# Kernel tuning notes

Measured on AMD Instinct MI355X. Metric: run time of the kernel, lower is better.

The kernel has to match this reference:

```python
import jax, jax.numpy as jnp
import numpy as np

NEG_SLOPE = 0.2  # PyG GATConv default negative_slope


def gat_conv(x, src, dst, n_nodes, W, a_src, a_dst, b, concat):
    # x: [N, F_in], W: [F_in, H*C], a_src/a_dst: [H, C], b: [H*C] or [C]
    H, C = a_src.shape
    h = (x @ W).reshape(n_nodes, H, C)              # [N, H, C]
    e_s = jnp.sum(h * a_src, axis=-1)               # [N, H]
    e_d = jnp.sum(h * a_dst, axis=-1)               # [N, H]
    e = jax.nn.leaky_relu(e_s[src] + e_d[dst], NEG_SLOPE)  # [E, H]
    # segment softmax over incoming edges of each destination node
    m = jax.ops.segment_max(e, dst, num_segments=n_nodes)
    m = jnp.where(jnp.isfinite(m), m, 0.0)
    p = jnp.exp(e - m[dst])                         # [E, H]
    s = jax.ops.segment_sum(p, dst, num_segments=n_nodes)
    alpha = p / (s[dst] + 1e-16)                    # [E, H]
    out = jax.ops.segment_sum(h[src] * alpha[:, :, None], dst, num_segments=n_nodes)  # [N, H, C]
    out = out.reshape(n_nodes, H * C) if concat else out.mean(axis=1)
    return out + b


def setup_inputs() -> dict:
    key = jax.random.key(0)
    ks = jax.random.split(key, 20)
    N, E = 50000, 800000
    F_in, C, H = 128, 64, 4
    sc = 0.05
    inp = {
        "x": jax.random.normal(ks[0], (N, F_in), dtype=jnp.float32),
        "edge_index": jax.random.randint(ks[1], (2, E), 0, N, dtype=jnp.int64),
        # conv1: F_in -> C x H heads, concat
        "W1": jax.random.normal(ks[2], (F_in, H * C), dtype=jnp.float32) * sc,
        "a1_src": jax.random.normal(ks[3], (H, C), dtype=jnp.float32) * sc,
        "a1_dst": jax.random.normal(ks[4], (H, C), dtype=jnp.float32) * sc,
        "b1": jnp.zeros((H * C,), dtype=jnp.float32),
        # conv2: H*C -> C x H heads, concat
        "W2": jax.random.normal(ks[5], (H * C, H * C), dtype=jnp.float32) * sc,
        "a2_src": jax.random.normal(ks[6], (H, C), dtype=jnp.float32) * sc,
        "a2_dst": jax.random.normal(ks[7], (H, C), dtype=jnp.float32) * sc,
        "b2": jnp.zeros((H * C,), dtype=jnp.float32),
        # conv3: H*C -> C, 1 head, concat=False (mean)
        "W3": jax.random.normal(ks[8], (H * C, C), dtype=jnp.float32) * sc,
        "a3_src": jax.random.normal(ks[9], (1, C), dtype=jnp.float32) * sc,
        "a3_dst": jax.random.normal(ks[10], (1, C), dtype=jnp.float32) * sc,
        "b3": jnp.zeros((C,), dtype=jnp.float32),
        # node classification head: C -> 2
        "cls_W": jax.random.normal(ks[11], (C, 2), dtype=jnp.float32) * sc,
        "cls_b": jnp.zeros((2,), dtype=jnp.float32),
    }
    return inp


def reference(x, edge_index, W1, a1_src, a1_dst, b1, W2, a2_src, a2_dst, b2,
              W3, a3_src, a3_dst, b3, cls_W, cls_b):
    N = x.shape[0]
    # PyG GATConv default: add self loops
    loop = jnp.arange(N, dtype=edge_index.dtype)
    ei = jnp.concatenate([edge_index, jnp.stack([loop, loop])], axis=1)
    src, dst = ei[0], ei[1]

    h = jax.nn.elu(gat_conv(x, src, dst, N, W1, a1_src, a1_dst, b1, concat=True))
    h = jax.nn.elu(gat_conv(h, src, dst, N, W2, a2_src, a2_dst, b2, concat=True))
    h = gat_conv(h, src, dst, N, W3, a3_src, a3_dst, b3, concat=False)  # [N, C]

    node_output = h @ cls_W + cls_b  # [N, 2]
    link_embedding = h               # [N, C]
    return node_output, link_embedding
```

## Files before the change

kernel.cpp:

```cpp
#include <hip/hip_runtime.h>
#include <math.h>


typedef unsigned short ushort;
typedef __attribute__((ext_vector_type(8))) short bf16x8;
typedef __attribute__((ext_vector_type(4))) float f32x4;

static __device__ __forceinline__ ushort f2bf(float f) {
    unsigned x = __float_as_uint(f);
    unsigned r = (x + 0x7FFF + ((x >> 16) & 1)) >> 16;
    return (ushort)r;
}
static __device__ __forceinline__ float bf2f(ushort u) {
    return __uint_as_float(((unsigned)u) << 16);
}


__global__ void count_deg(const int* __restrict__ ei, int E, int* __restrict__ deg) {
    int i = blockIdx.x * blockDim.x + threadIdx.x;
    int stride = gridDim.x * blockDim.x;
    for (int e = i; e < E; e += stride) {
        int d = ei[E + e];
        atomicAdd(&deg[d], 1);
    }
}

__global__ void scan_local(const int* __restrict__ deg, int* __restrict__ offsets,
                           int* __restrict__ blockSums, int N) {
    int tid = threadIdx.x;
    int lane = tid & 63;
    int wv = tid >> 6;
    int base = blockIdx.x * 1024 + tid * 4;
    int v[4];
#pragma unroll
    for (int j = 0; j < 4; ++j) {
        int idx = base + j;
        v[j] = (idx < N) ? (deg[idx] + 1) : 0;
    }
    int tsum = v[0] + v[1] + v[2] + v[3];
    int inc = tsum;
#pragma unroll
    for (int off = 1; off < 64; off <<= 1) {
        int u = __shfl_up(inc, off);
        if (lane >= off) inc += u;
    }
    __shared__ int wtot[4];
    if (lane == 63) wtot[wv] = inc;
    __syncthreads();
    int wbase = 0;
#pragma unroll
    for (int w = 0; w < 4; ++w)
        if (w < wv) wbase += wtot[w];
    int run = wbase + inc - tsum;
#pragma unroll
    for (int j = 0; j < 4; ++j) {
        int idx = base + j;
        if (idx < N) offsets[idx] = run;
        run += v[j];
    }
    if (tid == 255) blockSums[blockIdx.x] = wbase + inc;
}

__global__ void scan_blocks(const int* __restrict__ blockSums, int* __restrict__ blockBase,
                            int* __restrict__ offsets, int N, int nblk) {
    int lane = threadIdx.x & 63;
    int v = (lane < nblk) ? blockSums[lane] : 0;
    int inc = v;
#pragma unroll
    for (int off = 1; off < 64; off <<= 1) {
        int u = __shfl_up(inc, off);
        if (lane >= off) inc += u;
    }
    if (lane < nblk) blockBase[lane] = inc - v;
    if (lane == 63) offsets[N] = inc;
}

__global__ void scan_add(int* __restrict__ offsets, const int* __restrict__ blockBase, int N) {
    int i = blockIdx.x * blockDim.x + threadIdx.x;
    if (i < N) offsets[i] += blockBase[i >> 10];
}

__global__ void fill_self(const int* __restrict__ offsets, int* __restrict__ counter,
                          int* __restrict__ csr_src, int N) {
    int i = blockIdx.x * blockDim.x + threadIdx.x;
    if (i < N) {
        csr_src[offsets[i]] = i;
        counter[i] = 1;
    }
}

__global__ void fill_edges(const int* __restrict__ ei, int E,
                           const int* __restrict__ offsets, int* __restrict__ counter,
                           int* __restrict__ csr_src) {
    int i = blockIdx.x * blockDim.x + threadIdx.x;
    int stride = gridDim.x * blockDim.x;
    for (int e = i; e < E; e += stride) {
        int s = ei[e];
        int d = ei[E + e];
        int pos = offsets[d] + atomicAdd(&counter[d], 1);
        csr_src[pos] = s;
    }
}


__global__ void xsplit(const float* __restrict__ X, ushort* __restrict__ Xh,
                       ushort* __restrict__ Xl, int total4) {
    int i = blockIdx.x * blockDim.x + threadIdx.x;
    if (i >= total4) return;
    float4 v = *(const float4*)(X + (size_t)i * 4);
    ushort4 h, l;
    h.x = f2bf(v.x); l.x = f2bf(v.x - bf2f(h.x));
    h.y = f2bf(v.y); l.y = f2bf(v.y - bf2f(h.y));
    h.z = f2bf(v.z); l.z = f2bf(v.z - bf2f(h.z));
    h.w = f2bf(v.w); l.w = f2bf(v.w - bf2f(h.w));
    *(ushort4*)(Xh + (size_t)i * 4) = h;
    *(ushort4*)(Xl + (size_t)i * 4) = l;
}

__global__ void wtrans_bf(const float* __restrict__ W, ushort* __restrict__ Wt,
                          int K, int N) {
    int id = blockIdx.x * blockDim.x + threadIdx.x;
    if (id >= K * N) return;
    int k = id % K, n = id / K;
    Wt[id] = f2bf(W[(size_t)k * N + n]);
}


template<int BM, int BN, int WM, int WN>
__global__ __launch_bounds__(256) void gemm_mfma(const ushort* __restrict__ Ah,
                                                 const ushort* __restrict__ Al,
                                                 const ushort* __restrict__ Bh,
                                                 ushort* __restrict__ Cb,
                                                 int M, int N, int K) {
    constexpr int BK = 32, PAD = 8;
    constexpr int MI = BM / WM / 16;
    constexpr int NI = BN / WN / 16;
    __shared__ ushort As[2][BM][BK + PAD];
    __shared__ ushort Bs[BN][BK + PAD];

    int tid = threadIdx.x;
    int lane = tid & 63;
    int wid = tid >> 6;
    int fr = lane & 15;
    int fg = lane >> 4;
    int wm0 = (wid / WN) * (BM / WM);
    int wn0 = (wid % WN) * (BN / WN);
    int mBase = blockIdx.x * BM;
    int nBase = blockIdx.y * BN;

    f32x4 acc[MI][NI];
#pragma unroll
    for (int mi = 0; mi < MI; ++mi)
#pragma unroll
        for (int ni = 0; ni < NI; ++ni) acc[mi][ni] = (f32x4)0.0f;

    constexpr int ACH = BM * BK / 8;
    constexpr int BCH = BN * BK / 8;

    const int KI = K / BK;
    for (int t = 0; t < KI; ++t) {
        int k0 = t * BK;
#pragma unroll
        for (int q = tid; q < ACH; q += 256) {
            int row = q >> 2;
            int sl = (q & 3) * 8;
            int gm = mBase + row;
            if (gm >= M) gm = M - 1;
            size_t off = (size_t)gm * K + k0 + sl;
            *(bf16x8*)&As[0][row][sl] = *(const bf16x8*)(Ah + off);
            *(bf16x8*)&As[1][row][sl] = *(const bf16x8*)(Al + off);
        }
#pragma unroll
        for (int q = tid; q < BCH; q += 256) {
            int row = q >> 2;
            int sl = (q & 3) * 8;
            size_t off = (size_t)(nBase + row) * K + k0 + sl;
            *(bf16x8*)&Bs[row][sl] = *(const bf16x8*)(Bh + off);
        }
        __syncthreads();

        bf16x8 afh[MI], afl[MI], bfh[NI];
#pragma unroll
        for (int mi = 0; mi < MI; ++mi) {
            afh[mi] = *(const bf16x8*)&As[0][wm0 + mi * 16 + fr][fg * 8];
            afl[mi] = *(const bf16x8*)&As[1][wm0 + mi * 16 + fr][fg * 8];
        }
#pragma unroll
        for (int ni = 0; ni < NI; ++ni)
            bfh[ni] = *(const bf16x8*)&Bs[wn0 + ni * 16 + fr][fg * 8];
#pragma unroll
        for (int mi = 0; mi < MI; ++mi)
#pragma unroll
            for (int ni = 0; ni < NI; ++ni) {
                acc[mi][ni] = __builtin_amdgcn_mfma_f32_16x16x32_bf16(
                    afh[mi], bfh[ni], acc[mi][ni], 0, 0, 0);
                acc[mi][ni] = __builtin_amdgcn_mfma_f32_16x16x32_bf16(
                    afl[mi], bfh[ni], acc[mi][ni], 0, 0, 0);
            }
        __syncthreads();
    }

#pragma unroll
    for (int mi = 0; mi < MI; ++mi) {
#pragma unroll
        for (int j = 0; j < 4; ++j) {
            int gm = mBase + wm0 + mi * 16 + fg * 4 + j;
            if (gm >= M) continue;
#pragma unroll
            for (int ni = 0; ni < NI; ++ni) {
                int gn = nBase + wn0 + ni * 16 + fr;
                Cb[(size_t)gm * N + gn] = f2bf(acc[mi][ni][j]);
            }
        }
    }
}


template<int HC, int H>
__global__ void attn_coef(const ushort* __restrict__ hb,
                          const float* __restrict__ a_src,
                          const float* __restrict__ a_dst,
                          float* __restrict__ e_s, float* __restrict__ e_d, int N) {
    int wid = (int)((blockIdx.x * (size_t)blockDim.x + threadIdx.x) >> 6);
    int lane = threadIdx.x & 63;
    if (wid >= N) return;
    if constexpr (HC == 256) {
        ushort4 q = *(const ushort4*)(hb + (size_t)wid * 256 + lane * 4);
        float4 as = *(const float4*)(a_src + lane * 4);
        float4 ad = *(const float4*)(a_dst + lane * 4);
        float h0 = bf2f(q.x), h1 = bf2f(q.y), h2 = bf2f(q.z), h3 = bf2f(q.w);
        float ps = h0 * as.x + h1 * as.y + h2 * as.z + h3 * as.w;
        float pd = h0 * ad.x + h1 * ad.y + h2 * ad.z + h3 * ad.w;
#pragma unroll
        for (int off = 1; off <= 8; off <<= 1) {
            ps += __shfl_xor(ps, off);
            pd += __shfl_xor(pd, off);
        }
        if ((lane & 15) == 0) {
            int hd = lane >> 4;
            e_s[(size_t)wid * H + hd] = ps;
            e_d[(size_t)wid * H + hd] = pd;
        }
    } else {
        float hv = bf2f(hb[(size_t)wid * HC + lane]);
        float ps = hv * a_src[lane];
        float pd = hv * a_dst[lane];
#pragma unroll
        for (int off = 1; off <= 32; off <<= 1) {
            ps += __shfl_xor(ps, off);
            pd += __shfl_xor(pd, off);
        }
        if (lane == 0) {
            e_s[wid] = ps;
            e_d[wid] = pd;
        }
    }
}


template<int HC, int H, bool ELU, int U, bool SPLIT>
__global__ void aggregate(const ushort* __restrict__ hb,
                          const float* __restrict__ e_s, const float* __restrict__ e_d,
                          const int* __restrict__ offsets, const int* __restrict__ csr_src,
                          const float* __restrict__ bias,
                          float* __restrict__ out,
                          ushort* __restrict__ oh, ushort* __restrict__ ol, int N) {
    int wid = (int)((blockIdx.x * (size_t)blockDim.x + threadIdx.x) >> 6);
    int lane = threadIdx.x & 63;
    if (wid >= N) return;
    constexpr int VEC = HC / 64;
    constexpr int C = HC / H;
    constexpr int ROWSH = (HC == 256) ? 9 : 7;
    int hd = (lane * VEC) / C;
    float ed = e_d[(size_t)wid * H + hd];
    int beg = offsets[wid], end = offsets[wid + 1];
    const char* hbB = (const char*)hb;
    const char* esB = (const char*)e_s;
    unsigned laneOff = (unsigned)lane * (VEC * 2);

    float s = 0.0f;
    float acc[VEC];
#pragma unroll
    for (int j = 0; j < VEC; ++j) acc[j] = 0.0f;

    for (int k = beg; k < end; k += U) {
        int sidx[U];
#pragma unroll
        for (int u = 0; u < U; ++u) {
            int kk = k + u;
            kk = (kk < end) ? kk : end - 1;
            sidx[u] = csr_src[kk];
        }
        float e[U];
#pragma unroll
        for (int u = 0; u < U; ++u)
            e[u] = *(const float*)(esB + (((unsigned)(sidx[u] * H + hd)) << 2));
        ushort4 hv4[U];
        ushort  hv1[U];
        if constexpr (VEC == 4) {
#pragma unroll
            for (int u = 0; u < U; ++u)
                hv4[u] = *(const ushort4*)(hbB + (((unsigned)sidx[u]) << ROWSH) + laneOff);
        } else {
#pragma unroll
            for (int u = 0; u < U; ++u)
                hv1[u] = *(const ushort*)(hbB + (((unsigned)sidx[u]) << ROWSH) + laneOff);
        }
        float p[U];
        float psum = 0.0f;
#pragma unroll
        for (int u = 0; u < U; ++u) {
            float t = e[u] + ed;
            t = (t >= 0.0f) ? t : 0.2f * t;
            t = (k + u < end) ? t : -1e30f;
            p[u] = __expf(t);
            psum += p[u];
        }
        s += psum;
        if constexpr (VEC == 4) {
#pragma unroll
            for (int u = 0; u < U; ++u) {
                acc[0] += p[u] * bf2f(hv4[u].x);
                acc[1] += p[u] * bf2f(hv4[u].y);
                acc[2] += p[u] * bf2f(hv4[u].z);
                acc[3] += p[u] * bf2f(hv4[u].w);
            }
        } else {
#pragma unroll
            for (int u = 0; u < U; ++u) acc[0] += p[u] * bf2f(hv1[u]);
        }
    }
    float inv = 1.0f / (s + 1e-16f);
    float o[VEC];
#pragma unroll
    for (int j = 0; j < VEC; ++j) {
        int f = lane * VEC + j;
        o[j] = acc[j] * inv + bias[f];
        if constexpr (ELU) o[j] = (o[j] > 0.0f) ? o[j] : expm1f(o[j]);
    }
    if constexpr (SPLIT) {
        if constexpr (VEC == 4) {
            ushort4 h4, l4;
            h4.x = f2bf(o[0]); l4.x = f2bf(o[0] - bf2f(h4.x));
            h4.y = f2bf(o[1]); l4.y = f2bf(o[1] - bf2f(h4.y));
            h4.z = f2bf(o[2]); l4.z = f2bf(o[2] - bf2f(h4.z));
            h4.w = f2bf(o[3]); l4.w = f2bf(o[3] - bf2f(h4.w));
            *(ushort4*)(oh + (size_t)wid * HC + lane * 4) = h4;
            *(ushort4*)(ol + (size_t)wid * HC + lane * 4) = l4;
        } else {
            ushort h1 = f2bf(o[0]);
            oh[(size_t)wid * HC + lane] = h1;
            ol[(size_t)wid * HC + lane] = f2bf(o[0] - bf2f(h1));
        }
    } else {
#pragma unroll
        for (int j = 0; j < VEC; ++j)
            out[(size_t)wid * HC + lane * VEC + j] = o[j];
    }
}


__global__ void cls_head(const float* __restrict__ h3, const float* __restrict__ W,
                         const float* __restrict__ b, float* __restrict__ out, int N) {
    int wid = (int)((blockIdx.x * (size_t)blockDim.x + threadIdx.x) >> 6);
    int lane = threadIdx.x & 63;
    if (wid >= N) return;
    float v = h3[(size_t)wid * 64 + lane];
    float p0 = v * W[lane * 2 + 0];
    float p1 = v * W[lane * 2 + 1];
#pragma unroll
    for (int off = 1; off <= 32; off <<= 1) {
        p0 += __shfl_xor(p0, off);
        p1 += __shfl_xor(p1, off);
    }
    if (lane == 0) {
        out[(size_t)wid * 2 + 0] = p0 + b[0];
        out[(size_t)wid * 2 + 1] = p1 + b[1];
    }
}


extern "C" void kernel_launch(void* const* d_in, const int* in_sizes, int n_in,
                              void* d_out, int out_size, void* d_ws, size_t ws_size,
                              hipStream_t stream) {
    const float* x      = (const float*)d_in[0];
    const int*   ei     = (const int*)d_in[1];
    const float* W1     = (const float*)d_in[2];
    const float* a1_src = (const float*)d_in[3];
    const float* a1_dst = (const float*)d_in[4];
    const float* b1     = (const float*)d_in[5];
    const float* W2     = (const float*)d_in[6];
    const float* a2_src = (const float*)d_in[7];
    const float* a2_dst = (const float*)d_in[8];
    const float* b2     = (const float*)d_in[9];
    const float* W3     = (const float*)d_in[10];
    const float* a3_src = (const float*)d_in[11];
    const float* a3_dst = (const float*)d_in[12];
    const float* b3     = (const float*)d_in[13];
    const float* cls_W  = (const float*)d_in[14];
    const float* cls_b  = (const float*)d_in[15];

    const int N = in_sizes[0] / 128;
    const int E = in_sizes[1] / 2;
    const int ET = E + N;
    const int HC = 256;
    const int nScanBlk = (N + 1023) / 1024;

    char* w = (char*)d_ws;
    auto carve = [&](size_t bytes) {
        char* p = w;
        w += (bytes + 255) & ~(size_t)255;
        return p;
    };
    int*    deg     = (int*)   carve((size_t)N * 4);
    int*    counter = (int*)   carve((size_t)N * 4);
    int*    offsets = (int*)   carve((size_t)(N + 1) * 4);
    int*    csr_src = (int*)   carve((size_t)ET * 4);
    int*    blkSums = (int*)   carve((size_t)64 * 4);
    int*    blkBase = (int*)   carve((size_t)64 * 4);
    float*  e_s     = (float*) carve((size_t)N * 4 * 4);
    float*  e_d     = (float*) carve((size_t)N * 4 * 4);
    ushort* hb      = (ushort*)carve((size_t)N * HC * 2);
    ushort* Ahi     = (ushort*)carve((size_t)N * HC * 2);
    ushort* Alo     = (ushort*)carve((size_t)N * HC * 2);
    ushort* W1t     = (ushort*)carve((size_t)128 * 256 * 2);
    ushort* W2t     = (ushort*)carve((size_t)256 * 256 * 2);
    ushort* W3t     = (ushort*)carve((size_t)256 * 64 * 2);
    (void)ws_size;

    float* out_node = (float*)d_out;
    float* out_link = (float*)d_out + 2 * (size_t)N;

    hipMemsetAsync(deg, 0, (size_t)N * 4, stream);
    int eblocks = (E + 255) / 256;
    if (eblocks > 2048) eblocks = 2048;
    count_deg<<<eblocks, 256, 0, stream>>>(ei, E, deg);
    scan_local<<<nScanBlk, 256, 0, stream>>>(deg, offsets, blkSums, N);
    scan_blocks<<<1, 64, 0, stream>>>(blkSums, blkBase, offsets, N, nScanBlk);
    scan_add<<<(N + 255) / 256, 256, 0, stream>>>(offsets, blkBase, N);
    fill_self<<<(N + 255) / 256, 256, 0, stream>>>(offsets, counter, csr_src, N);
    fill_edges<<<eblocks, 256, 0, stream>>>(ei, E, offsets, counter, csr_src);

    xsplit<<<(N * 128 / 4 + 255) / 256, 256, 0, stream>>>(x, Ahi, Alo, N * 128 / 4);
    wtrans_bf<<<(128 * 256 + 255) / 256, 256, 0, stream>>>(W1, W1t, 128, 256);
    wtrans_bf<<<(256 * 256 + 255) / 256, 256, 0, stream>>>(W2, W2t, 256, 256);
    wtrans_bf<<<(256 * 64 + 255) / 256, 256, 0, stream>>>(W3, W3t, 256, 64);

    dim3 g12((N + 63) / 64, 1);
    dim3 g3((N + 63) / 64, 1);
    int nodeBlocks = (N + 3) / 4;

    gemm_mfma<64, 256, 1, 4><<<g12, 256, 0, stream>>>(Ahi, Alo, W1t, hb, N, 256, 128);
    attn_coef<256, 4><<<nodeBlocks, 256, 0, stream>>>(hb, a1_src, a1_dst, e_s, e_d, N);
    aggregate<256, 4, true, 8, true><<<nodeBlocks, 256, 0, stream>>>(
        hb, e_s, e_d, offsets, csr_src, b1, nullptr, Ahi, Alo, N);
    gemm_mfma<64, 256, 1, 4><<<g12, 256, 0, stream>>>(Ahi, Alo, W2t, hb, N, 256, 256);
    attn_coef<256, 4><<<nodeBlocks, 256, 0, stream>>>(hb, a2_src, a2_dst, e_s, e_d, N);
    aggregate<256, 4, true, 8, true><<<nodeBlocks, 256, 0, stream>>>(
        hb, e_s, e_d, offsets, csr_src, b2, nullptr, Ahi, Alo, N);
    gemm_mfma<64, 64, 2, 2><<<g3, 256, 0, stream>>>(Ahi, Alo, W3t, hb, N, 64, 256);
    attn_coef<64, 1><<<nodeBlocks, 256, 0, stream>>>(hb, a3_src, a3_dst, e_s, e_d, N);
    aggregate<64, 1, false, 8, false><<<nodeBlocks, 256, 0, stream>>>(
        hb, e_s, e_d, offsets, csr_src, b3, out_link, nullptr, nullptr, N);
    cls_head<<<nodeBlocks, 256, 0, stream>>>(out_link, cls_W, cls_b, out_node, N);
}
```

Measured before the change: 388.6 us.

## Pad CSR rows to multiples of 8 with sentinel node and use exp2

After: 372.9 us. -4.0%, faster.

```diff
diff --git a/kernel.cpp b/kernel.cpp
--- a/kernel.cpp
+++ b/kernel.cpp
@@ -5,6 +5,8 @@
 typedef unsigned short ushort;
 typedef __attribute__((ext_vector_type(8))) short bf16x8;
 typedef __attribute__((ext_vector_type(4))) float f32x4;
+
+#define LOG2E 1.4426950408889634f
 
 static __device__ __forceinline__ ushort f2bf(float f) {
     unsigned x = __float_as_uint(f);
@@ -35,7 +37,7 @@
 #pragma unroll
     for (int j = 0; j < 4; ++j) {
         int idx = base + j;
-        v[j] = (idx < N) ? (deg[idx] + 1) : 0;
+        v[j] = (idx < N) ? ((deg[idx] + 1 + 7) & ~7) : 0;
     }
     int tsum = v[0] + v[1] + v[2] + v[3];
     int inc = tsum;
@@ -78,6 +80,11 @@
 __global__ void scan_add(int* __restrict__ offsets, const int* __restrict__ blockBase, int N) {
     int i = blockIdx.x * blockDim.x + threadIdx.x;
     if (i < N) offsets[i] += blockBase[i >> 10];
+}
+
+__global__ void fill_sent(int* __restrict__ csr_src, int cap, int N) {
+    int i = blockIdx.x * blockDim.x + threadIdx.x;
+    if (i < cap) csr_src[i] = N;
 }
 
 __global__ void fill_self(const int* __restrict__ offsets, int* __restrict__ counter,
@@ -126,15 +133,16 @@
 }
 
 
-template<int BM, int BN, int WM, int WN>
-__global__ __launch_bounds__(256) void gemm_mfma(const ushort* __restrict__ Ah,
-                                                 const ushort* __restrict__ Al,
-                                                 const ushort* __restrict__ Bh,
-                                                 ushort* __restrict__ Cb,
-                                                 int M, int N, int K) {
+template<int BM, int BN, int WM, int WN, int THREADS>
+__global__ __launch_bounds__(THREADS) void gemm_mfma(const ushort* __restrict__ Ah,
+                                                     const ushort* __restrict__ Al,
+                                                     const ushort* __restrict__ Bh,
+                                                     ushort* __restrict__ Cb,
+                                                     int M, int N, int K) {
     constexpr int BK = 32, PAD = 8;
     constexpr int MI = BM / WM / 16;
     constexpr int NI = BN / WN / 16;
+    static_assert(WM * WN * 64 == THREADS, "wave grid mismatch");
     __shared__ ushort As[2][BM][BK + PAD];
     __shared__ ushort Bs[BN][BK + PAD];
 
@@ -160,8 +168,7 @@
     const int KI = K / BK;
     for (int t = 0; t < KI; ++t) {
         int k0 = t * BK;
-#pragma unroll
-        for (int q = tid; q < ACH; q += 256) {
+        for (int q = tid; q < ACH; q += THREADS) {
             int row = q >> 2;
             int sl = (q & 3) * 8;
             int gm = mBase + row;
@@ -170,8 +177,7 @@
             *(bf16x8*)&As[0][row][sl] = *(const bf16x8*)(Ah + off);
             *(bf16x8*)&As[1][row][sl] = *(const bf16x8*)(Al + off);
         }
-#pragma unroll
-        for (int q = tid; q < BCH; q += 256) {
+        for (int q = tid; q < BCH; q += THREADS) {
             int row = q >> 2;
             int sl = (q & 3) * 8;
             size_t off = (size_t)(nBase + row) * K + k0 + sl;
@@ -217,13 +223,23 @@
 
 
 template<int HC, int H>
-__global__ void attn_coef(const ushort* __restrict__ hb,
+__global__ void attn_coef(ushort* __restrict__ hb,
                           const float* __restrict__ a_src,
                           const float* __restrict__ a_dst,
                           float* __restrict__ e_s, float* __restrict__ e_d, int N) {
     int wid = (int)((blockIdx.x * (size_t)blockDim.x + threadIdx.x) >> 6);
     int lane = threadIdx.x & 63;
-    if (wid >= N) return;
+    if (wid > N) return;
+    if (wid == N) {
+        if constexpr (HC == 256) {
+            ushort4 z = {0, 0, 0, 0};
+            *(ushort4*)(hb + (size_t)N * 256 + lane * 4) = z;
+        } else {
+            hb[(size_t)N * HC + lane] = 0;
+        }
+        if (lane < H) e_s[(size_t)N * H + lane] = -1e30f;
+        return;
+    }
     if constexpr (HC == 256) {
         ushort4 q = *(const ushort4*)(hb + (size_t)wid * 256 + lane * 4);
         float4 as = *(const float4*)(a_src + lane * 4);
@@ -238,8 +254,8 @@
         }
         if ((lane & 15) == 0) {
             int hd = lane >> 4;
-            e_s[(size_t)wid * H + hd] = ps;
-            e_d[(size_t)wid * H + hd] = pd;
+            e_s[(size_t)wid * H + hd] = ps * LOG2E;
+            e_d[(size_t)wid * H + hd] = pd * LOG2E;
         }
     } else {
         float hv = bf2f(hb[(size_t)wid * HC + lane]);
@@ -251,20 +267,21 @@
             pd += __shfl_xor(pd, off);
         }
         if (lane == 0) {
-            e_s[wid] = ps;
-            e_d[wid] = pd;
-        }
-    }
-}
-
-
-template<int HC, int H, bool ELU, int U, bool SPLIT>
+            e_s[wid] = ps * LOG2E;
+            e_d[wid] = pd * LOG2E;
+        }
+    }
+}
+
+
+template<int HC, int H, bool ELU, bool SPLIT>
 __global__ void aggregate(const ushort* __restrict__ hb,
                           const float* __restrict__ e_s, const float* __restrict__ e_d,
                           const int* __restrict__ offsets, const int* __restrict__ csr_src,
                           const float* __restrict__ bias,
                           float* __restrict__ out,
                           ushort* __restrict__ oh, ushort* __restrict__ ol, int N) {
+    constexpr int U = 8;
     int wid = (int)((blockIdx.x * (size_t)blockDim.x + threadIdx.x) >> 6);
     int lane = threadIdx.x & 63;
     if (wid >= N) return;
@@ -286,11 +303,7 @@
     for (int k = beg; k < end; k += U) {
         int sidx[U];
 #pragma unroll
-        for (int u = 0; u < U; ++u) {
-            int kk = k + u;
-            kk = (kk < end) ? kk : end - 1;
-            sidx[u] = csr_src[kk];
-        }
+        for (int u = 0; u < U; ++u) sidx[u] = csr_src[k + u];
         float e[U];
 #pragma unroll
         for (int u = 0; u < U; ++u)
@@ -312,8 +325,7 @@
         for (int u = 0; u < U; ++u) {
             float t = e[u] + ed;
             t = (t >= 0.0f) ? t : 0.2f * t;
-            t = (k + u < end) ? t : -1e30f;
-            p[u] = __expf(t);
+            p[u] = __builtin_amdgcn_exp2f(t);
             psum += p[u];
         }
         s += psum;
@@ -402,7 +414,7 @@
 
     const int N = in_sizes[0] / 128;
     const int E = in_sizes[1] / 2;
-    const int ET = E + N;
+    const int ETcap = E + 8 * N + 64;
     const int HC = 256;
     const int nScanBlk = (N + 1023) / 1024;
 
@@ -415,12 +427,12 @@
     int*    deg     = (int*)   carve((size_t)N * 4);
     int*    counter = (int*)   carve((size_t)N * 4);
     int*    offsets = (int*)   carve((size_t)(N + 1) * 4);
-    int*    csr_src = (int*)   carve((size_t)ET * 4);
+    int*    csr_src = (int*)   carve((size_t)ETcap * 4);
     int*    blkSums = (int*)   carve((size_t)64 * 4);
     int*    blkBase = (int*)   carve((size_t)64 * 4);
-    float*  e_s     = (float*) carve((size_t)N * 4 * 4);
+    float*  e_s     = (float*) carve((size_t)(N + 1) * 4 * 4);
     float*  e_d     = (float*) carve((size_t)N * 4 * 4);
-    ushort* hb      = (ushort*)carve((size_t)N * HC * 2);
+    ushort* hb      = (ushort*)carve((size_t)(N + 1) * HC * 2);
     ushort* Ahi     = (ushort*)carve((size_t)N * HC * 2);
     ushort* Alo     = (ushort*)carve((size_t)N * HC * 2);
     ushort* W1t     = (ushort*)carve((size_t)128 * 256 * 2);
@@ -438,6 +450,7 @@
     scan_local<<<nScanBlk, 256, 0, stream>>>(deg, offsets, blkSums, N);
     scan_blocks<<<1, 64, 0, stream>>>(blkSums, blkBase, offsets, N, nScanBlk);
     scan_add<<<(N + 255) / 256, 256, 0, stream>>>(offsets, blkBase, N);
+    fill_sent<<<(ETcap + 255) / 256, 256, 0, stream>>>(csr_src, ETcap, N);
     fill_self<<<(N + 255) / 256, 256, 0, stream>>>(offsets, counter, csr_src, N);
     fill_edges<<<eblocks, 256, 0, stream>>>(ei, E, offsets, counter, csr_src);
 
@@ -448,19 +461,20 @@
 
     dim3 g12((N + 63) / 64, 1);
     dim3 g3((N + 63) / 64, 1);
-    int nodeBlocks = (N + 3) / 4;
-
-    gemm_mfma<64, 256, 1, 4><<<g12, 256, 0, stream>>>(Ahi, Alo, W1t, hb, N, 256, 128);
-    attn_coef<256, 4><<<nodeBlocks, 256, 0, stream>>>(hb, a1_src, a1_dst, e_s, e_d, N);
-    aggregate<256, 4, true, 8, true><<<nodeBlocks, 256, 0, stream>>>(
+    int nodeBlocks  = (N + 3) / 4;
+    int nodeBlocksP = (N + 1 + 3) / 4;
+
+    gemm_mfma<64, 256, 2, 4, 512><<<g12, 512, 0, stream>>>(Ahi, Alo, W1t, hb, N, 256, 128);
+    attn_coef<256, 4><<<nodeBlocksP, 256, 0, stream>>>(hb, a1_src, a1_dst, e_s, e_d, N);
+    aggregate<256, 4, true, true><<<nodeBlocks, 256, 0, stream>>>(
         hb, e_s, e_d, offsets, csr_src, b1, nullptr, Ahi, Alo, N);
-    gemm_mfma<64, 256, 1, 4><<<g12, 256, 0, stream>>>(Ahi, Alo, W2t, hb, N, 256, 256);
-    attn_coef<256, 4><<<nodeBlocks, 256, 0, stream>>>(hb, a2_src, a2_dst, e_s, e_d, N);
-    aggregate<256, 4, true, 8, true><<<nodeBlocks, 256, 0, stream>>>(
+    gemm_mfma<64, 256, 2, 4, 512><<<g12, 512, 0, stream>>>(Ahi, Alo, W2t, hb, N, 256, 256);
+    attn_coef<256, 4><<<nodeBlocksP, 256, 0, stream>>>(hb, a2_src, a2_dst, e_s, e_d, N);
+    aggregate<256, 4, true, true><<<nodeBlocks, 256, 0, stream>>>(
         hb, e_s, e_d, offsets, csr_src, b2, nullptr, Ahi, Alo, N);
-    gemm_mfma<64, 64, 2, 2><<<g3, 256, 0, stream>>>(Ahi, Alo, W3t, hb, N, 64, 256);
-    attn_coef<64, 1><<<nodeBlocks, 256, 0, stream>>>(hb, a3_src, a3_dst, e_s, e_d, N);
-    aggregate<64, 1, false, 8, false><<<nodeBlocks, 256, 0, stream>>>(
+    gemm_mfma<64, 64, 4, 2, 512><<<g3, 512, 0, stream>>>(Ahi, Alo, W3t, hb, N, 64, 256);
+    attn_coef<64, 1><<<nodeBlocksP, 256, 0, stream>>>(hb, a3_src, a3_dst, e_s, e_d, N);
+    aggregate<64, 1, false, false><<<nodeBlocks, 256, 0, stream>>>(
         hb, e_s, e_d, offsets, csr_src, b3, out_link, nullptr, nullptr, N);
     cls_head<<<nodeBlocks, 256, 0, stream>>>(out_link, cls_W, cls_b, out_node, N);
 }
```
